# Kernel tuning notes

Measured on AMD Instinct MI355X. Metric: run time of the kernel, lower is better.

## Reference

```python
import jax, jax.numpy as jnp
import numpy as np

N_NODES = 100000
N_EDGES = 1600000
C_IN = 128
C_HID = 128
C_OUT = 128


def _gcn_conv(x, row, col, ew, W, b, n_nodes):
    # PyG GCNConv with edge weights and self-loops already included in (row, col, ew).
    # deg[i] = sum of edge weights into node i (flow source->target, aggregate at col)
    xw = x @ W                                                # [N, C_out]
    deg = jax.ops.segment_sum(ew, col, num_segments=n_nodes)  # [N]
    dinv = jnp.where(deg > 0, jax.lax.rsqrt(deg), 0.0)        # deg^{-1/2}, inf -> 0
    norm = dinv[row] * ew * dinv[col]                         # [E]
    msg = xw[row] * norm[:, None]                             # gather + scale
    out = jax.ops.segment_sum(msg, col, num_segments=n_nodes) # scatter-add
    return out + b


def setup_inputs() -> dict:
    key = jax.random.key(0)
    ks = jax.random.split(key, 10)
    x = jax.random.normal(ks[0], (N_NODES, C_IN), dtype=jnp.float32)
    edge_index = jax.random.randint(ks[1], (2, N_EDGES), 0, N_NODES, dtype=jnp.int32)
    edge_weight = jax.random.uniform(ks[2], (N_EDGES,), dtype=jnp.float32)
    s = 1.0 / np.sqrt(C_HID)
    W1 = jax.random.uniform(ks[3], (C_IN, C_HID), minval=-s, maxval=s, dtype=jnp.float32)
    b1 = jnp.zeros((C_HID,), dtype=jnp.float32)
    W2 = jax.random.uniform(ks[4], (C_HID, C_HID), minval=-s, maxval=s, dtype=jnp.float32)
    b2 = jnp.zeros((C_HID,), dtype=jnp.float32)
    W3 = jax.random.uniform(ks[5], (C_HID, C_OUT), minval=-s, maxval=s, dtype=jnp.float32)
    b3 = jnp.zeros((C_OUT,), dtype=jnp.float32)
    return {"x": x, "edge_index": edge_index, "edge_weight": edge_weight,
            "W1": W1, "b1": b1, "W2": W2, "b2": b2, "W3": W3, "b3": b3}


def reference(x, edge_index, edge_weight, W1, b1, W2, b2, W3, b3):
    n = x.shape[0]
    # add self-loops with weight 1 (PyG add_self_loops; identical each layer, built once)
    loop = jnp.arange(n, dtype=edge_index.dtype)
    row = jnp.concatenate([edge_index[0], loop])
    col = jnp.concatenate([edge_index[1], loop])
    ew = jnp.concatenate([edge_weight, jnp.ones((n,), dtype=edge_weight.dtype)])
    h = _gcn_conv(x, row, col, ew, W1, b1, n)
    h = jax.nn.relu(h)
    h = _gcn_conv(h, row, col, ew, W2, b2, n)
    h = jax.nn.relu(h)
    h = _gcn_conv(h, row, col, ew, W3, b3, n)
    return h
```

## Files before the change

### kernel.cpp

```cpp
#include <hip/hip_runtime.h>

#define NN 100000
#define NE 1600000

typedef __attribute__((ext_vector_type(8))) short short8;
typedef __attribute__((ext_vector_type(4))) float f32x4;

static __device__ __forceinline__ unsigned f2bf_rne(float f) {
    unsigned u = __float_as_uint(f);
    return (u + 0x7FFFu + ((u >> 16) & 1u)) >> 16;
}
static __device__ __forceinline__ float bf_lo(unsigned u) { return __uint_as_float(u << 16); }
static __device__ __forceinline__ float bf_hi(unsigned u) { return __uint_as_float(u & 0xFFFF0000u); }

__global__ __launch_bounds__(256) void k_init(unsigned long long* packed, int n) {
    int i = blockIdx.x * 256 + threadIdx.x;
    if (i < n) packed[(size_t)i << 4] = 0ull;
}

__global__ __launch_bounds__(256) void k_prep(const float* __restrict__ W,
                                              ushort* __restrict__ Wth,
                                              ushort* __restrict__ Wtl) {
    int idx = blockIdx.x * 256 + threadIdx.x;
    int k = idx >> 7, n = idx & 127;
    float w = W[idx];
    unsigned hi = f2bf_rne(w);
    unsigned lo = f2bf_rne(w - bf_lo(hi));
    Wth[n * 128 + k] = (ushort)hi;
    Wtl[n * 128 + k] = (ushort)lo;
}

template <bool SPLIT_A>
static __device__ __forceinline__ void mfma_tile(const ushort* sAh, const ushort* sAl,
                                                 const ushort* __restrict__ Wth,
                                                 const ushort* __restrict__ Wtl,
                                                 unsigned* __restrict__ Cb,
                                                 size_t r0, int t) {
    int w  = t >> 6;
    int l  = t & 63;
    int lr = l & 15;
    int lk = (l >> 4) << 3;
    int n0 = w * 32;

    short8 bh[2][4], bl[2][4];
#pragma unroll
    for (int cf = 0; cf < 2; ++cf)
#pragma unroll
        for (int ks = 0; ks < 4; ++ks) {
            int n = n0 + cf * 16 + lr;
            bh[cf][ks] = *(const short8*)&Wth[n * 128 + ks * 32 + lk];
            bl[cf][ks] = *(const short8*)&Wtl[n * 128 + ks * 32 + lk];
        }

    f32x4 zero = {0.f, 0.f, 0.f, 0.f};
    f32x4 acc[2][2] = {{zero, zero}, {zero, zero}};

    __syncthreads();

#pragma unroll
    for (int ks = 0; ks < 4; ++ks) {
        short8 ah[2], al[2];
#pragma unroll
        for (int rf = 0; rf < 2; ++rf) {
            int off = (rf * 16 + lr) * 136 + ks * 32 + lk;
            ah[rf] = *(const short8*)&sAh[off];
            if (SPLIT_A) al[rf] = *(const short8*)&sAl[off];
        }
#pragma unroll
        for (int rf = 0; rf < 2; ++rf)
#pragma unroll
            for (int cf = 0; cf < 2; ++cf) {
                acc[rf][cf] = __builtin_amdgcn_mfma_f32_16x16x32_bf16(ah[rf], bh[cf][ks], acc[rf][cf], 0, 0, 0);
                acc[rf][cf] = __builtin_amdgcn_mfma_f32_16x16x32_bf16(ah[rf], bl[cf][ks], acc[rf][cf], 0, 0, 0);
                if (SPLIT_A)
                    acc[rf][cf] = __builtin_amdgcn_mfma_f32_16x16x32_bf16(al[rf], bh[cf][ks], acc[rf][cf], 0, 0, 0);
            }
    }

#pragma unroll
    for (int rf = 0; rf < 2; ++rf)
#pragma unroll
        for (int cf = 0; cf < 2; ++cf)
#pragma unroll
            for (int r = 0; r < 4; ++r) {
                unsigned b = f2bf_rne(acc[rf][cf][r]);
                unsigned p = (unsigned)__shfl_xor((int)b, 1);
                if (!(l & 1)) {
                    size_t row = r0 + rf * 16 + ((l >> 4) << 2) + r;
                    int c = n0 + cf * 16 + lr;
                    Cb[(row * 128 + c) >> 1] = b | (p << 16);
                }
            }
}

__global__ __launch_bounds__(256) void k_gp(const float* __restrict__ A,
                                            const ushort* __restrict__ Wth,
                                            const ushort* __restrict__ Wtl,
                                            unsigned* __restrict__ Cb,
                                            const int* __restrict__ col,
                                            const float* __restrict__ ew,
                                            unsigned long long* packed,
                                            int* __restrict__ rank, int e) {
    __shared__ alignas(16) ushort sAh[32 * 136];
    __shared__ alignas(16) ushort sAl[32 * 136];
    int b = blockIdx.x;
    int sub = b % 3;
    int q = b / 3;
    int t = threadIdx.x;

    if (sub != 0) {
        int p = q * 2 + sub - 1;
        int i = p * 256 + t;
        if (i < e) {
            int c = col[i];
            unsigned fe = (unsigned)__float2uint_rn(ew[i] * 1048576.0f);
            unsigned long long inc = ((unsigned long long)fe << 24) | 1ull;
            unsigned long long old = atomicAdd(&packed[(size_t)c << 4], inc);
            rank[i] = (int)(old & 0xFFFFFFull);
        }
        return;
    }

    size_t r0 = (size_t)q * 32;
    const float4* A4 = (const float4*)(A + r0 * 128);
#pragma unroll
    for (int i = 0; i < 4; ++i) {
        int j = t + 256 * i;
        float4 f = A4[j];
        int rr = j >> 5;
        int cc = (j & 31) << 2;
        unsigned h0 = f2bf_rne(f.x), h1 = f2bf_rne(f.y), h2 = f2bf_rne(f.z), h3 = f2bf_rne(f.w);
        unsigned g0 = f2bf_rne(f.x - bf_lo(h0)), g1 = f2bf_rne(f.y - bf_lo(h1));
        unsigned g2 = f2bf_rne(f.z - bf_lo(h2)), g3 = f2bf_rne(f.w - bf_lo(h3));
        *(ushort4*)&sAh[rr * 136 + cc] = make_ushort4((ushort)h0, (ushort)h1, (ushort)h2, (ushort)h3);
        *(ushort4*)&sAl[rr * 136 + cc] = make_ushort4((ushort)g0, (ushort)g1, (ushort)g2, (ushort)g3);
    }
    mfma_tile<true>(sAh, sAl, Wth, Wtl, Cb, r0, t);
}

__global__ __launch_bounds__(256) void k_scan1(const unsigned long long* __restrict__ packed,
                                               int* __restrict__ rowptr,
                                               int* __restrict__ part,
                                               float* __restrict__ dinv, int n) {
    __shared__ int s[256];
    int t = threadIdx.x;
    int i = blockIdx.x * 256 + t;
    unsigned long long pk = (i < n) ? packed[(size_t)i << 4] : 0ull;
    int v = (int)(pk & 0xFFFFFFull);
    if (i < n) {
        float deg = 1.0f + (float)(pk >> 24) * (1.0f / 1048576.0f);
        dinv[i] = rsqrtf(deg);
    }
    s[t] = v;
    __syncthreads();
    for (int d = 1; d < 256; d <<= 1) {
        int y = (t >= d) ? s[t - d] : 0;
        __syncthreads();
        s[t] += y;
        __syncthreads();
    }
    if (i < n) rowptr[i] = s[t] - v;
    if (t == 255) part[blockIdx.x] = s[255];
}

__global__ __launch_bounds__(512) void k_scan2(int* part, int m) {
    __shared__ int s[512];
    int t = threadIdx.x;
    int v = (t < m) ? part[t] : 0;
    s[t] = v;
    __syncthreads();
    for (int d = 1; d < 512; d <<= 1) {
        int y = (t >= d) ? s[t - d] : 0;
        __syncthreads();
        s[t] += y;
        __syncthreads();
    }
    if (t < m) part[t] = s[t] - v;
}

__global__ __launch_bounds__(256) void k_scan3(int* rowptr, const int* __restrict__ part, int n, int e) {
    int i = blockIdx.x * 256 + threadIdx.x;
    if (i < n) rowptr[i] += part[blockIdx.x];
    if (i == 0) rowptr[n] = e;
}

__global__ __launch_bounds__(256) void k_fill(const int* __restrict__ row,
                                              const int* __restrict__ col,
                                              const float* __restrict__ ew,
                                              const int* __restrict__ rowptr,
                                              const int* __restrict__ rank,
                                              const float* __restrict__ dinv,
                                              uint2* __restrict__ meta, int e) {
    int i = blockIdx.x * 256 + threadIdx.x;
    if (i < e) {
        int c = col[i];
        int r = row[i];
        int p = rowptr[c] + rank[i];
        float w = dinv[r] * ew[i] * dinv[c];
        meta[p] = make_uint2((unsigned)r, __float_as_uint(w));
    }
}

__global__ __launch_bounds__(256) void k_gemm_b(const unsigned* __restrict__ Ab,
                                                const ushort* __restrict__ Wth,
                                                const ushort* __restrict__ Wtl,
                                                unsigned* __restrict__ Cb) {
    __shared__ alignas(16) ushort sA[32 * 136];
    int t = threadIdx.x;
    size_t r0 = (size_t)blockIdx.x * 32;

    const uint4* A4 = (const uint4*)(Ab + r0 * 64);
#pragma unroll
    for (int i = 0; i < 2; ++i) {
        int j = t + 256 * i;
        uint4 u = A4[j];
        int rr = j >> 4;
        int cc = (j & 15) << 3;
        *(uint4*)&sA[rr * 136 + cc] = u;
    }
    mfma_tile<false>(sA, nullptr, Wth, Wtl, Cb, r0, t);
}

__global__ __launch_bounds__(256) void k_agg(const unsigned* __restrict__ XWb,
                                             const int* __restrict__ rowptr,
                                             const uint2* __restrict__ meta,
                                             const float* __restrict__ dinv,
                                             const float* __restrict__ bias,
                                             unsigned* __restrict__ outb,
                                             float* __restrict__ outf, int relu, int n) {
    int lane = threadIdx.x & 63;
    int node = blockIdx.x * 4 + (threadIdx.x >> 6);
    if (node >= n) return;

    float di = dinv[node];
    float selfw = di * di;
    unsigned uself = XWb[(size_t)node * 64 + lane];
    float2 bv = *(const float2*)(bias + lane * 2);
    float ax = fmaf(selfw, bf_lo(uself), bv.x);
    float ay = fmaf(selfw, bf_hi(uself), bv.y);

    int p0 = rowptr[node], p1 = rowptr[node + 1];
    for (int base = p0; base < p1; base += 64) {
        int m = p1 - base; if (m > 64) m = 64;
        int idx = base + (lane < m ? lane : m - 1);
        uint2 mv = meta[idx];
        int sv = (int)mv.x;
        float wv = __uint_as_float(mv.y);
        int j = 0;
        for (; j + 8 <= m; j += 8) {
            int s0 = __shfl(sv, j),     s1 = __shfl(sv, j + 1);
            int s2 = __shfl(sv, j + 2), s3 = __shfl(sv, j + 3);
            int s4 = __shfl(sv, j + 4), s5 = __shfl(sv, j + 5);
            int s6 = __shfl(sv, j + 6), s7 = __shfl(sv, j + 7);
            float w0 = __shfl(wv, j),     w1 = __shfl(wv, j + 1);
            float w2 = __shfl(wv, j + 2), w3 = __shfl(wv, j + 3);
            float w4 = __shfl(wv, j + 4), w5 = __shfl(wv, j + 5);
            float w6 = __shfl(wv, j + 6), w7 = __shfl(wv, j + 7);
            unsigned u0 = XWb[(size_t)s0 * 64 + lane];
            unsigned u1 = XWb[(size_t)s1 * 64 + lane];
            unsigned u2 = XWb[(size_t)s2 * 64 + lane];
            unsigned u3 = XWb[(size_t)s3 * 64 + lane];
            unsigned u4 = XWb[(size_t)s4 * 64 + lane];
            unsigned u5 = XWb[(size_t)s5 * 64 + lane];
            unsigned u6 = XWb[(size_t)s6 * 64 + lane];
            unsigned u7 = XWb[(size_t)s7 * 64 + lane];
            ax = fmaf(w0, bf_lo(u0), ax);  ay = fmaf(w0, bf_hi(u0), ay);
            ax = fmaf(w1, bf_lo(u1), ax);  ay = fmaf(w1, bf_hi(u1), ay);
            ax = fmaf(w2, bf_lo(u2), ax);  ay = fmaf(w2, bf_hi(u2), ay);
            ax = fmaf(w3, bf_lo(u3), ax);  ay = fmaf(w3, bf_hi(u3), ay);
            ax = fmaf(w4, bf_lo(u4), ax);  ay = fmaf(w4, bf_hi(u4), ay);
            ax = fmaf(w5, bf_lo(u5), ax);  ay = fmaf(w5, bf_hi(u5), ay);
            ax = fmaf(w6, bf_lo(u6), ax);  ay = fmaf(w6, bf_hi(u6), ay);
            ax = fmaf(w7, bf_lo(u7), ax);  ay = fmaf(w7, bf_hi(u7), ay);
        }
        for (; j + 4 <= m; j += 4) {
            int s0 = __shfl(sv, j),     s1 = __shfl(sv, j + 1);
            int s2 = __shfl(sv, j + 2), s3 = __shfl(sv, j + 3);
            float w0 = __shfl(wv, j),     w1 = __shfl(wv, j + 1);
            float w2 = __shfl(wv, j + 2), w3 = __shfl(wv, j + 3);
            unsigned u0 = XWb[(size_t)s0 * 64 + lane];
            unsigned u1 = XWb[(size_t)s1 * 64 + lane];
            unsigned u2 = XWb[(size_t)s2 * 64 + lane];
            unsigned u3 = XWb[(size_t)s3 * 64 + lane];
            ax = fmaf(w0, bf_lo(u0), ax);  ay = fmaf(w0, bf_hi(u0), ay);
            ax = fmaf(w1, bf_lo(u1), ax);  ay = fmaf(w1, bf_hi(u1), ay);
            ax = fmaf(w2, bf_lo(u2), ax);  ay = fmaf(w2, bf_hi(u2), ay);
            ax = fmaf(w3, bf_lo(u3), ax);  ay = fmaf(w3, bf_hi(u3), ay);
        }
        for (; j < m; ++j) {
            int s = __shfl(sv, j);
            float w = __shfl(wv, j);
            unsigned u = XWb[(size_t)s * 64 + lane];
            ax = fmaf(w, bf_lo(u), ax);
            ay = fmaf(w, bf_hi(u), ay);
        }
    }
    if (relu) {
        ax = fmaxf(ax, 0.0f);
        ay = fmaxf(ay, 0.0f);
        outb[(size_t)node * 64 + lane] = f2bf_rne(ax) | (f2bf_rne(ay) << 16);
    } else {
        *(float2*)(outf + (size_t)node * 128 + lane * 2) = make_float2(ax, ay);
    }
}

extern "C" void kernel_launch(void* const* d_in, const int* in_sizes, int n_in,
                              void* d_out, int out_size, void* d_ws, size_t ws_size,
                              hipStream_t stream) {
    const float* x  = (const float*)d_in[0];
    const int*   ei = (const int*)d_in[1];
    const float* ew = (const float*)d_in[2];
    const float* W1 = (const float*)d_in[3];
    const float* b1 = (const float*)d_in[4];
    const float* W2 = (const float*)d_in[5];
    const float* b2 = (const float*)d_in[6];
    const float* W3 = (const float*)d_in[7];
    const float* b3 = (const float*)d_in[8];
    float* out = (float*)d_out;

    const int n = NN, e = NE;
    const int* row = ei;
    const int* col = ei + e;

    char* ws = (char*)d_ws;
    size_t off = 0;
    auto alloc = [&](size_t bytes) -> void* {
        void* p = ws + off;
        off = (off + bytes + 255) & ~(size_t)255;
        return p;
    };
    unsigned*           hb     = (unsigned*)alloc((size_t)n * 128 * 2);
    unsigned*           xwb    = (unsigned*)alloc((size_t)n * 128 * 2);
    void*               uni    =            alloc((size_t)n * 16 * 8);
    unsigned long long* packed = (unsigned long long*)uni;
    uint2*              meta   = (uint2*)uni;
    float*              dinv   = (float*)   alloc((size_t)n * 4);
    int*                rowptr = (int*)     alloc((size_t)(n + 1) * 4);
    int*                rank   = (int*)     alloc((size_t)e * 4);
    int*                part   = (int*)     alloc(512 * 4);
    ushort*             wt     = (ushort*)  alloc(6 * 16384 * 2);
    (void)ws_size; (void)in_sizes; (void)n_in; (void)out_size;

    int nb = (n + 255) / 256;
    int eb = (e + 255) / 256;
    int gb = n / 32;
    int ab = (n + 3) / 4;

    k_init<<<nb, 256, 0, stream>>>(packed, n);
    k_prep<<<64, 256, 0, stream>>>(W1, wt + 0 * 16384, wt + 1 * 16384);
    k_prep<<<64, 256, 0, stream>>>(W2, wt + 2 * 16384, wt + 3 * 16384);
    k_prep<<<64, 256, 0, stream>>>(W3, wt + 4 * 16384, wt + 5 * 16384);

    k_gp<<<gb + eb, 256, 0, stream>>>(x, wt + 0 * 16384, wt + 1 * 16384, xwb, col, ew, packed, rank, e);
    k_scan1<<<nb, 256, 0, stream>>>(packed, rowptr, part, dinv, n);
    k_scan2<<<1, 512, 0, stream>>>(part, nb);
    k_scan3<<<nb, 256, 0, stream>>>(rowptr, part, n, e);
    k_fill<<<eb, 256, 0, stream>>>(row, col, ew, rowptr, rank, dinv, meta, e);

    k_agg<<<ab, 256, 0, stream>>>(xwb, rowptr, meta, dinv, b1, hb, (float*)nullptr, 1, n);
    k_gemm_b<<<gb, 256, 0, stream>>>(hb, wt + 2 * 16384, wt + 3 * 16384, xwb);
    k_agg<<<ab, 256, 0, stream>>>(xwb, rowptr, meta, dinv, b2, hb, (float*)nullptr, 1, n);
    k_gemm_b<<<gb, 256, 0, stream>>>(hb, wt + 4 * 16384, wt + 5 * 16384, xwb);
    k_agg<<<ab, 256, 0, stream>>>(xwb, rowptr, meta, dinv, b3, (unsigned*)nullptr, out, 0, n);
}
```

Baseline: 495.4 us.

## Process two nodes per wavefront in aggregation with 8-byte feature loads

The aggregation kernel now maps two destination nodes onto each 64-lane wavefront: each half-wave handles one node, and every lane loads 8 bytes (four bf16 features) per neighbour instead of 4 bytes. Neighbour metadata is read in chunks of 32 per half, and both halves loop to the larger of the two degrees, with padded iterations masked to zero weight. The aim is fewer, wider gather instructions and fewer shuffle and loop iterations per edge. In exchange, work diverges when the two nodes' degrees differ, adding wasted gathers and longer serial chains per lane.

```diff
diff --git a/kernel.cpp b/kernel.cpp
--- a/kernel.cpp
+++ b/kernel.cpp
@@ -229,78 +229,69 @@
                                              unsigned* __restrict__ outb,
                                              float* __restrict__ outf, int relu, int n) {
     int lane = threadIdx.x & 63;
-    int node = blockIdx.x * 4 + (threadIdx.x >> 6);
+    int h = lane >> 5;
+    int q = lane & 31;
+    int node = blockIdx.x * 8 + ((threadIdx.x >> 6) << 1) + h;
     if (node >= n) return;
 
+    const uint2* X2 = (const uint2*)XWb;
     float di = dinv[node];
     float selfw = di * di;
-    unsigned uself = XWb[(size_t)node * 64 + lane];
-    float2 bv = *(const float2*)(bias + lane * 2);
-    float ax = fmaf(selfw, bf_lo(uself), bv.x);
-    float ay = fmaf(selfw, bf_hi(uself), bv.y);
+    uint2 us = X2[(size_t)node * 32 + q];
+    float4 bv = *(const float4*)(bias + q * 4);
+    float a0 = fmaf(selfw, bf_lo(us.x), bv.x);
+    float a1 = fmaf(selfw, bf_hi(us.x), bv.y);
+    float a2 = fmaf(selfw, bf_lo(us.y), bv.z);
+    float a3 = fmaf(selfw, bf_hi(us.y), bv.w);
 
     int p0 = rowptr[node], p1 = rowptr[node + 1];
-    for (int base = p0; base < p1; base += 64) {
-        int m = p1 - base; if (m > 64) m = 64;
-        int idx = base + (lane < m ? lane : m - 1);
+    int deg = p1 - p0;
+    int dmax = max(deg, __shfl_xor(deg, 32));
+
+    for (int base = 0; base < dmax; base += 32) {
+        int m = deg - base;
+        if (m > 32) m = 32;
+        int mm = dmax - base;
+        if (mm > 32) mm = 32;
+        int idx = p0 + base + (q < m ? q : (m > 0 ? m - 1 : 0));
+        if (m <= 0) idx = p0;
+        if (idx > NE - 1) idx = NE - 1;
         uint2 mv = meta[idx];
         int sv = (int)mv.x;
         float wv = __uint_as_float(mv.y);
+
         int j = 0;
-        for (; j + 8 <= m; j += 8) {
-            int s0 = __shfl(sv, j),     s1 = __shfl(sv, j + 1);
-            int s2 = __shfl(sv, j + 2), s3 = __shfl(sv, j + 3);
-            int s4 = __shfl(sv, j + 4), s5 = __shfl(sv, j + 5);
-            int s6 = __shfl(sv, j + 6), s7 = __shfl(sv, j + 7);
-            float w0 = __shfl(wv, j),     w1 = __shfl(wv, j + 1);
-            float w2 = __shfl(wv, j + 2), w3 = __shfl(wv, j + 3);
-            float w4 = __shfl(wv, j + 4), w5 = __shfl(wv, j + 5);
-            float w6 = __shfl(wv, j + 6), w7 = __shfl(wv, j + 7);
-            unsigned u0 = XWb[(size_t)s0 * 64 + lane];
-            unsigned u1 = XWb[(size_t)s1 * 64 + lane];
-            unsigned u2 = XWb[(size_t)s2 * 64 + lane];
-            unsigned u3 = XWb[(size_t)s3 * 64 + lane];
-            unsigned u4 = XWb[(size_t)s4 * 64 + lane];
-            unsigned u5 = XWb[(size_t)s5 * 64 + lane];
-            unsigned u6 = XWb[(size_t)s6 * 64 + lane];
-            unsigned u7 = XWb[(size_t)s7 * 64 + lane];
-            ax = fmaf(w0, bf_lo(u0), ax);  ay = fmaf(w0, bf_hi(u0), ay);
-            ax = fmaf(w1, bf_lo(u1), ax);  ay = fmaf(w1, bf_hi(u1), ay);
-            ax = fmaf(w2, bf_lo(u2), ax);  ay = fmaf(w2, bf_hi(u2), ay);
-            ax = fmaf(w3, bf_lo(u3), ax);  ay = fmaf(w3, bf_hi(u3), ay);
-            ax = fmaf(w4, bf_lo(u4), ax);  ay = fmaf(w4, bf_hi(u4), ay);
-            ax = fmaf(w5, bf_lo(u5), ax);  ay = fmaf(w5, bf_hi(u5), ay);
-            ax = fmaf(w6, bf_lo(u6), ax);  ay = fmaf(w6, bf_hi(u6), ay);
-            ax = fmaf(w7, bf_lo(u7), ax);  ay = fmaf(w7, bf_hi(u7), ay);
-        }
-        for (; j + 4 <= m; j += 4) {
-            int s0 = __shfl(sv, j),     s1 = __shfl(sv, j + 1);
-            int s2 = __shfl(sv, j + 2), s3 = __shfl(sv, j + 3);
-            float w0 = __shfl(wv, j),     w1 = __shfl(wv, j + 1);
-            float w2 = __shfl(wv, j + 2), w3 = __shfl(wv, j + 3);
-            unsigned u0 = XWb[(size_t)s0 * 64 + lane];
-            unsigned u1 = XWb[(size_t)s1 * 64 + lane];
-            unsigned u2 = XWb[(size_t)s2 * 64 + lane];
-            unsigned u3 = XWb[(size_t)s3 * 64 + lane];
-            ax = fmaf(w0, bf_lo(u0), ax);  ay = fmaf(w0, bf_hi(u0), ay);
-            ax = fmaf(w1, bf_lo(u1), ax);  ay = fmaf(w1, bf_hi(u1), ay);
-            ax = fmaf(w2, bf_lo(u2), ax);  ay = fmaf(w2, bf_hi(u2), ay);
-            ax = fmaf(w3, bf_lo(u3), ax);  ay = fmaf(w3, bf_hi(u3), ay);
-        }
-        for (; j < m; ++j) {
-            int s = __shfl(sv, j);
-            float w = __shfl(wv, j);
-            unsigned u = XWb[(size_t)s * 64 + lane];
-            ax = fmaf(w, bf_lo(u), ax);
-            ay = fmaf(w, bf_hi(u), ay);
-        }
-    }
+        for (; j + 4 <= mm; j += 4) {
+#pragma unroll
+            for (int u = 0; u < 4; ++u) {
+                int jj = j + u;
+                int s = __shfl(sv, (h << 5) | jj);
+                float w = __shfl(wv, (h << 5) | jj);
+                w = (jj < m) ? w : 0.0f;
+                uint2 u0 = X2[(size_t)s * 32 + q];
+                a0 = fmaf(w, bf_lo(u0.x), a0);  a1 = fmaf(w, bf_hi(u0.x), a1);
+                a2 = fmaf(w, bf_lo(u0.y), a2);  a3 = fmaf(w, bf_hi(u0.y), a3);
+            }
+        }
+        for (; j < mm; ++j) {
+            int s = __shfl(sv, (h << 5) | j);
+            float w = __shfl(wv, (h << 5) | j);
+            w = (j < m) ? w : 0.0f;
+            uint2 u0 = X2[(size_t)s * 32 + q];
+            a0 = fmaf(w, bf_lo(u0.x), a0);  a1 = fmaf(w, bf_hi(u0.x), a1);
+            a2 = fmaf(w, bf_lo(u0.y), a2);  a3 = fmaf(w, bf_hi(u0.y), a3);
+        }
+    }
+
     if (relu) {
-        ax = fmaxf(ax, 0.0f);
-        ay = fmaxf(ay, 0.0f);
-        outb[(size_t)node * 64 + lane] = f2bf_rne(ax) | (f2bf_rne(ay) << 16);
+        a0 = fmaxf(a0, 0.0f);  a1 = fmaxf(a1, 0.0f);
+        a2 = fmaxf(a2, 0.0f);  a3 = fmaxf(a3, 0.0f);
+        uint2 o;
+        o.x = f2bf_rne(a0) | (f2bf_rne(a1) << 16);
+        o.y = f2bf_rne(a2) | (f2bf_rne(a3) << 16);
+        ((uint2*)outb)[(size_t)node * 32 + q] = o;
     } else {
-        *(float2*)(outf + (size_t)node * 128 + lane * 2) = make_float2(ax, ay);
+        *(float4*)(outf + (size_t)node * 128 + q * 4) = make_float4(a0, a1, a2, a3);
     }
 }
 
@@ -344,7 +335,7 @@
     int nb = (n + 255) / 256;
     int eb = (e + 255) / 256;
     int gb = n / 32;
-    int ab = (n + 3) / 4;
+    int ab = (n + 7) / 8;
 
     k_init<<<nb, 256, 0, stream>>>(packed, n);
     k_prep<<<64, 256, 0, stream>>>(W1, wt + 0 * 16384, wt + 1 * 16384);
```

Measured after the change: 490.4 us. About the same (-1.0%).
